# Kernel optimization log

Hardware: AMD Instinct MI355X
Metric: run time of the kernel (lower is better)

The kernel has to match this reference:

```python
import jax, jax.numpy as jnp
import numpy as np

K = 20  # number of top neighbors kept per row
NOISE_SCALE = 1e-4


def setup_inputs() -> dict:
    key = jax.random.key(0)
    k1, k2 = jax.random.split(key)
    B, N = 16, 2048
    A = jax.random.normal(k1, (B, N, N), dtype=jnp.float32)
    noise = jax.random.uniform(k2, (B, N, N), dtype=jnp.float32)
    return {"A": A, "noise": noise}


def reference(A, noise):
    # _activate: ReLU
    A = jax.nn.relu(A)

    # _sparsify: per-row top-k on noise-doped scores, scatter a 0/1 mask, multiply
    A_doped = A + noise * NOISE_SCALE
    _, topk_idx = jax.lax.top_k(A_doped, K)  # (B, N, K)
    B, N, _ = A.shape
    b_idx = jnp.arange(B)[:, None, None]
    r_idx = jnp.arange(N)[None, :, None]
    mask = jnp.zeros_like(A).at[b_idx, r_idx, topk_idx].set(1.0)
    A = A * mask

    # _symmetrize
    A = (A + jnp.swapaxes(A, 1, 2)) * 0.5

    # _normalize ('sym'): A <- D^{-1/2} (A + I) D^{-1/2}
    A = A + jnp.eye(N, dtype=A.dtype)
    d_inv = jnp.sum(A, axis=2) ** -0.5  # (B, N)
    d_inv = jnp.where(jnp.isinf(d_inv), 0.0, d_inv)
    # diag(d) @ A @ diag(d) expressed via broadcasting (same math as batched matmul)
    A = d_inv[:, :, None] * A * d_inv[:, None, :]
    return A
```

## Files before the change

### kernel.cpp

```cpp
#include <hip/hip_runtime.h>

#define NN 2048
#define KK 20
#define BB 16
#define T0F 1.8f
#define CAP 128
#define CSLOT 64

typedef __attribute__((ext_vector_type(4))) float f32x4;

__global__ __launch_bounds__(256, 4) void topk_kernel(
    const float* __restrict__ A, const float* __restrict__ noise,
    int* __restrict__ sel_idx, float* __restrict__ sel_val,
    float* __restrict__ colsum, int* __restrict__ col_cnt,
    unsigned short* __restrict__ col_src)
{
    __shared__ float cand_key[4][CAP];
    __shared__ float cand_val[4][CAP];
    __shared__ int   cand_idx[4][CAP];
    __shared__ int   tie_idx[4][64];
    __shared__ int   tie_cnt[4];

    const int lane = threadIdx.x & 63;
    const int wv   = threadIdx.x >> 6;
    const int row  = blockIdx.x * 4 + wv;
    const float* Ar = A     + (size_t)row * NN;
    const float* Nr = noise + (size_t)row * NN;
    const int colbase = row & ~(NN - 1);
    const unsigned long long ltm = (1ull << lane) - 1ull;

    int*   si = sel_idx + (size_t)row * KK;
    float* sv = sel_val + (size_t)row * KK;

#define EMIT(POS, IDX, V)                                                      \
    do {                                                                       \
        int _p = (POS); int _i = (IDX); float _v = (V);                        \
        si[_p] = _i; sv[_p] = _v;                                              \
        atomicAdd(&colsum[colbase + _i], _v);                                  \
        int _s = atomicAdd(&col_cnt[colbase + _i], 1);                         \
        if (_s < CSLOT)                                                        \
            col_src[(size_t)(colbase + _i) * CSLOT + _s] =                     \
                (unsigned short)(((row & (NN - 1)) << 5) | _p);                \
    } while (0)

    float4 a[8], z[8];
#pragma unroll
    for (int c = 0; c < 8; ++c) a[c] = *(const float4*)(Ar + c * 256 + lane * 4);
#pragma unroll
    for (int c = 0; c < 8; ++c) z[c] = *(const float4*)(Nr + c * 256 + lane * 4);

    int cnt = 0;
#pragma unroll
    for (int c = 0; c < 8; ++c) {
        float av[4] = {a[c].x, a[c].y, a[c].z, a[c].w};
        float nv[4] = {z[c].x, z[c].y, z[c].z, z[c].w};
#pragma unroll
        for (int q = 0; q < 4; ++q) {
            float v = fmaxf(av[q], 0.f);
            float k = v + nv[q] * 1e-4f;
            bool p = k >= T0F;
            unsigned long long m = __ballot(p);
            if (p) {
                int pos = cnt + __popcll(m & ltm);
                if (pos < CAP) {
                    cand_key[wv][pos] = k;
                    cand_val[wv][pos] = v;
                    cand_idx[wv][pos] = c * 256 + lane * 4 + q;
                }
            }
            cnt += __popcll(m);
        }
    }

    bool done = false;
    if (cnt == KK) {
        if (lane < KK)
            EMIT(lane, cand_idx[wv][lane], cand_val[wv][lane]);
        done = true;
    } else if (cnt > KK && cnt <= CAP) {
        float c0 = (lane      < cnt) ? cand_key[wv][lane]      : -1.f;
        float c1 = (lane + 64 < cnt) ? cand_key[wv][lane + 64] : -1.f;

        float mx = fmaxf(c0, c1);
#pragma unroll
        for (int s = 32; s; s >>= 1) mx = fmaxf(mx, __shfl_xor(mx, s));

        unsigned lo = __float_as_uint(T0F);
        unsigned hi = __float_as_uint(mx) + 1u;
        bool exact = false; unsigned tb = 0;
        while (hi - lo > 1u) {
            unsigned mid = (lo + hi) >> 1;
            float tm = __uint_as_float(mid);
            int c = __popcll(__ballot(c0 >= tm)) + __popcll(__ballot(c1 >= tm));
            if (c == KK) { tb = mid; exact = true; break; }
            if (c > KK) lo = mid; else hi = mid;
        }
        if (exact) {
            float t = __uint_as_float(tb);
            bool p = c0 >= t;
            unsigned long long m = __ballot(p);
            if (p) EMIT(__popcll(m & ltm), cand_idx[wv][lane], cand_val[wv][lane]);
            int run = __popcll(m);
            p = c1 >= t;
            m = __ballot(p);
            if (p) EMIT(run + __popcll(m & ltm), cand_idx[wv][lane + 64],
                        cand_val[wv][lane + 64]);
            done = true;
        }
    }

    if (!done) {
        unsigned lo = 0u, hi = 0x7F800000u;
        unsigned tb = 0u;
        bool exact = false;
        while (hi - lo > 1u) {
            unsigned mid = (lo + hi) >> 1;
            float tm = __uint_as_float(mid);
            int c = 0;
            for (int j = 0; j < 32; ++j) {
                float av = Ar[j * 64 + lane];
                float nv = Nr[j * 64 + lane];
                float k = fmaxf(av, 0.f) + nv * 1e-4f;
                c += __popcll(__ballot(k >= tm));
            }
            if (c == KK) { tb = mid; exact = true; break; }
            if (c > KK) lo = mid; else hi = mid;
        }
        if (exact) {
            float t = __uint_as_float(tb);
            int run = 0;
            for (int j = 0; j < 32; ++j) {
                float av = Ar[j * 64 + lane];
                float nv = Nr[j * 64 + lane];
                float v = fmaxf(av, 0.f);
                float k = v + nv * 1e-4f;
                bool p = k >= t;
                unsigned long long m = __ballot(p);
                if (p) EMIT(run + __popcll(m & ltm), j * 64 + lane, v);
                run += __popcll(m);
            }
        } else {
            float t1 = __uint_as_float(lo);
            int run = 0;
            for (int j = 0; j < 32; ++j) {
                float av = Ar[j * 64 + lane];
                float nv = Nr[j * 64 + lane];
                float v = fmaxf(av, 0.f);
                float k = v + nv * 1e-4f;
                bool p = k > t1;
                unsigned long long m = __ballot(p);
                if (p) EMIT(run + __popcll(m & ltm), j * 64 + lane, v);
                run += __popcll(m);
            }
            if (lane == 0) tie_cnt[wv] = 0;
            for (int j = 0; j < 32; ++j) {
                float av = Ar[j * 64 + lane];
                float nv = Nr[j * 64 + lane];
                float k = fmaxf(av, 0.f) + nv * 1e-4f;
                if (k == t1) {
                    int p = atomicAdd(&tie_cnt[wv], 1);
                    if (p < 64) tie_idx[wv][p] = j * 64 + lane;
                }
            }
            if (lane == 0) {
                int n = tie_cnt[wv]; if (n > 64) n = 64;
                int need = KK - run;
                for (int s = 0; s < need; ++s) {
                    int bq = 0, bidx = 0x7fffffff;
                    for (int q = 0; q < n; ++q) {
                        int v = tie_idx[wv][q];
                        if (v < bidx) { bidx = v; bq = q; }
                    }
                    tie_idx[wv][bq] = 0x7fffffff;
                    float v = fmaxf(Ar[bidx], 0.f);
                    EMIT(run + s, bidx, v);
                }
            }
        }
    }
#undef EMIT
}

__global__ __launch_bounds__(256) void dinv_kernel(
    const float* __restrict__ sel_val, const float* __restrict__ colsum,
    float* __restrict__ dinv)
{
    int r = blockIdx.x * 256 + threadIdx.x;
    const float* svp = sel_val + (size_t)r * KK;
    float rs = 0.f;
#pragma unroll
    for (int k = 0; k < KK; ++k) rs += svp[k];
    float d = 1.0f + 0.5f * (rs + colsum[r]);
    dinv[r] = 1.0f / sqrtf(d);
}

__global__ __launch_bounds__(256) void dense_row_kernel(
    const int* __restrict__ sel_idx, const float* __restrict__ sel_val,
    const int* __restrict__ col_cnt, const unsigned short* __restrict__ col_src,
    const float* __restrict__ dinv, float* __restrict__ out)
{
    __shared__ float rowbuf[NN];
    const int r = blockIdx.x;
    const int i = r & (NN - 1);
    const int t = threadIdx.x;
    const int colbase = r & ~(NN - 1);

    float4 zz = {0.f, 0.f, 0.f, 0.f};
#pragma unroll
    for (int c = 0; c < 2; ++c)
        *(float4*)(rowbuf + c * 1024 + t * 4) = zz;
    __syncthreads();

    float di = dinv[r];
    if (t == 0) atomicAdd(&rowbuf[i], di * di);
    if (t < KK) {
        int j  = sel_idx[(size_t)r * KK + t];
        float v = sel_val[(size_t)r * KK + t];
        atomicAdd(&rowbuf[j], 0.5f * v * di * dinv[colbase + j]);
    }
    int cnt = col_cnt[r]; if (cnt > CSLOT) cnt = CSLOT;
    if (t < cnt) {
        unsigned short pk = col_src[(size_t)r * CSLOT + t];
        int srow = pk >> 5, k = pk & 31;
        float v = sel_val[(size_t)(colbase + srow) * KK + k];
        atomicAdd(&rowbuf[srow], 0.5f * v * di * dinv[colbase + srow]);
    }
    __syncthreads();

    size_t base = (size_t)r * NN;
#pragma unroll
    for (int c = 0; c < 2; ++c) {
        int col = c * 1024 + t * 4;
        f32x4 v = *(const f32x4*)(rowbuf + col);
        __builtin_nontemporal_store(v, (f32x4*)(out + base + col));
    }
}

extern "C" void kernel_launch(void* const* d_in, const int* in_sizes, int n_in,
                              void* d_out, int out_size, void* d_ws, size_t ws_size,
                              hipStream_t stream)
{
    const float* A     = (const float*)d_in[0];
    const float* noise = (const float*)d_in[1];
    float* out = (float*)d_out;
    char*  ws  = (char*)d_ws;

    const int rows = BB * NN;
    size_t off = 0;
    int*   sel_idx = (int*)(ws + off);            off += (size_t)rows * KK * 4;
    float* sel_val = (float*)(ws + off);          off += (size_t)rows * KK * 4;
    float* colsum  = (float*)(ws + off);          off += (size_t)rows * 4;
    float* dinv    = (float*)(ws + off);          off += (size_t)rows * 4;
    int*   col_cnt = (int*)(ws + off);            off += (size_t)rows * 4;
    unsigned short* col_src = (unsigned short*)(ws + off);

    hipMemsetAsync(colsum, 0, rows * sizeof(float), stream);
    hipMemsetAsync(col_cnt, 0, rows * sizeof(int), stream);

    topk_kernel<<<rows / 4, 256, 0, stream>>>(A, noise, sel_idx, sel_val,
                                              colsum, col_cnt, col_src);
    dinv_kernel<<<rows / 256, 256, 0, stream>>>(sel_val, colsum, dinv);
    dense_row_kernel<<<rows, 256, 0, stream>>>(sel_idx, sel_val, col_cnt,
                                               col_src, dinv, out);
}
```

Baseline: 700.8 us.

## Prefilter top-k on A alone, gather noise lazily, and batch rows per block

The top-k kernel now screens candidates using only relu(A) against a slightly lowered threshold. It reads noise just for the few surviving indices instead of streaming the whole noise row, which roughly halves the dense input bytes. Each wave handles four rows and prefetches the next row's A while finishing the current one. The dense output kernel processes eight rows per block to amortise launch and setup cost. Candidate compaction now uses LDS atomics, so candidate order is no longer deterministic, and the lowered prefilter threshold must still capture every key above the cutoff.

```diff
diff --git a/kernel.cpp b/kernel.cpp
--- a/kernel.cpp
+++ b/kernel.cpp
@@ -4,33 +4,44 @@
 #define KK 20
 #define BB 16
 #define T0F 1.8f
+#define TPRE (T0F - 1.1e-4f)
 #define CAP 128
 #define CSLOT 64
+#define RPW 4
+#define DRROWS 8
 
 typedef __attribute__((ext_vector_type(4))) float f32x4;
 
-__global__ __launch_bounds__(256, 4) void topk_kernel(
+__global__ __launch_bounds__(256) void topk_kernel(
     const float* __restrict__ A, const float* __restrict__ noise,
     int* __restrict__ sel_idx, float* __restrict__ sel_val,
     float* __restrict__ colsum, int* __restrict__ col_cnt,
     unsigned short* __restrict__ col_src)
 {
-    __shared__ float cand_key[4][CAP];
+    __shared__ int   cand_idx[4][CAP];
     __shared__ float cand_val[4][CAP];
-    __shared__ int   cand_idx[4][CAP];
+    __shared__ int   cand_cnt[4];
     __shared__ int   tie_idx[4][64];
     __shared__ int   tie_cnt[4];
 
     const int lane = threadIdx.x & 63;
     const int wv   = threadIdx.x >> 6;
-    const int row  = blockIdx.x * 4 + wv;
-    const float* Ar = A     + (size_t)row * NN;
-    const float* Nr = noise + (size_t)row * NN;
-    const int colbase = row & ~(NN - 1);
     const unsigned long long ltm = (1ull << lane) - 1ull;
 
-    int*   si = sel_idx + (size_t)row * KK;
-    float* sv = sel_val + (size_t)row * KK;
+    if (lane == 0) cand_cnt[wv] = 0;
+
+    int base = 0;
+
+    {
+        const float* Ar0 = A + (size_t)(blockIdx.x * (4 * RPW) + wv) * NN;
+    }
+    float4 a[8];
+    {
+        const float* Ar0 = A + (size_t)(blockIdx.x * (4 * RPW) + wv) * NN;
+#pragma unroll
+        for (int c = 0; c < 8; ++c)
+            a[c] = *(const float4*)(Ar0 + c * 256 + lane * 4);
+    }
 
 #define EMIT(POS, IDX, V)                                                      \
     do {                                                                       \
@@ -43,137 +54,161 @@
                 (unsigned short)(((row & (NN - 1)) << 5) | _p);                \
     } while (0)
 
-    float4 a[8], z[8];
-#pragma unroll
-    for (int c = 0; c < 8; ++c) a[c] = *(const float4*)(Ar + c * 256 + lane * 4);
-#pragma unroll
-    for (int c = 0; c < 8; ++c) z[c] = *(const float4*)(Nr + c * 256 + lane * 4);
-
-    int cnt = 0;
-#pragma unroll
-    for (int c = 0; c < 8; ++c) {
-        float av[4] = {a[c].x, a[c].y, a[c].z, a[c].w};
-        float nv[4] = {z[c].x, z[c].y, z[c].z, z[c].w};
-#pragma unroll
-        for (int q = 0; q < 4; ++q) {
-            float v = fmaxf(av[q], 0.f);
-            float k = v + nv[q] * 1e-4f;
-            bool p = k >= T0F;
-            unsigned long long m = __ballot(p);
-            if (p) {
-                int pos = cnt + __popcll(m & ltm);
-                if (pos < CAP) {
-                    cand_key[wv][pos] = k;
-                    cand_val[wv][pos] = v;
-                    cand_idx[wv][pos] = c * 256 + lane * 4 + q;
+#pragma unroll
+    for (int rr = 0; rr < RPW; ++rr) {
+        const int row = blockIdx.x * (4 * RPW) + rr * 4 + wv;
+        const float* Ar = A     + (size_t)row * NN;
+        const float* Nr = noise + (size_t)row * NN;
+        const int colbase = row & ~(NN - 1);
+        int*   si = sel_idx + (size_t)row * KK;
+        float* sv = sel_val + (size_t)row * KK;
+
+        int mycnt = 0;
+#pragma unroll
+        for (int c = 0; c < 8; ++c) {
+            float av[4] = {a[c].x, a[c].y, a[c].z, a[c].w};
+#pragma unroll
+            for (int q = 0; q < 4; ++q) {
+                float v = fmaxf(av[q], 0.f);
+                if (v >= TPRE) {
+                    int p = atomicAdd(&cand_cnt[wv], 1) - base;
+                    if (p < CAP) {
+                        cand_idx[wv][p] = c * 256 + lane * 4 + q;
+                        cand_val[wv][p] = v;
+                    }
+                    ++mycnt;
                 }
             }
-            cnt += __popcll(m);
-        }
-    }
-
-    bool done = false;
-    if (cnt == KK) {
-        if (lane < KK)
-            EMIT(lane, cand_idx[wv][lane], cand_val[wv][lane]);
-        done = true;
-    } else if (cnt > KK && cnt <= CAP) {
-        float c0 = (lane      < cnt) ? cand_key[wv][lane]      : -1.f;
-        float c1 = (lane + 64 < cnt) ? cand_key[wv][lane + 64] : -1.f;
-
-        float mx = fmaxf(c0, c1);
-#pragma unroll
-        for (int s = 32; s; s >>= 1) mx = fmaxf(mx, __shfl_xor(mx, s));
-
-        unsigned lo = __float_as_uint(T0F);
-        unsigned hi = __float_as_uint(mx) + 1u;
-        bool exact = false; unsigned tb = 0;
-        while (hi - lo > 1u) {
-            unsigned mid = (lo + hi) >> 1;
-            float tm = __uint_as_float(mid);
-            int c = __popcll(__ballot(c0 >= tm)) + __popcll(__ballot(c1 >= tm));
-            if (c == KK) { tb = mid; exact = true; break; }
-            if (c > KK) lo = mid; else hi = mid;
-        }
-        if (exact) {
-            float t = __uint_as_float(tb);
-            bool p = c0 >= t;
-            unsigned long long m = __ballot(p);
-            if (p) EMIT(__popcll(m & ltm), cand_idx[wv][lane], cand_val[wv][lane]);
-            int run = __popcll(m);
-            p = c1 >= t;
-            m = __ballot(p);
-            if (p) EMIT(run + __popcll(m & ltm), cand_idx[wv][lane + 64],
-                        cand_val[wv][lane + 64]);
-            done = true;
-        }
-    }
-
-    if (!done) {
-        unsigned lo = 0u, hi = 0x7F800000u;
-        unsigned tb = 0u;
-        bool exact = false;
-        while (hi - lo > 1u) {
-            unsigned mid = (lo + hi) >> 1;
-            float tm = __uint_as_float(mid);
-            int c = 0;
-            for (int j = 0; j < 32; ++j) {
-                float av = Ar[j * 64 + lane];
-                float nv = Nr[j * 64 + lane];
-                float k = fmaxf(av, 0.f) + nv * 1e-4f;
-                c += __popcll(__ballot(k >= tm));
+        }
+
+        if (rr + 1 < RPW) {
+            const float* An = A + (size_t)(row + 4) * NN;
+#pragma unroll
+            for (int c = 0; c < 8; ++c)
+                a[c] = *(const float4*)(An + c * 256 + lane * 4);
+        }
+
+        int cnt = mycnt;
+#pragma unroll
+        for (int s = 32; s; s >>= 1) cnt += __shfl_xor(cnt, s);
+        base += cnt;
+
+        bool done = false;
+        if (cnt <= CAP) {
+            int   i0 = (lane      < cnt) ? cand_idx[wv][lane]      : -1;
+            int   i1 = (lane + 64 < cnt) ? cand_idx[wv][lane + 64] : -1;
+            float v0 = (i0 >= 0) ? cand_val[wv][lane]      : 0.f;
+            float v1 = (i1 >= 0) ? cand_val[wv][lane + 64] : 0.f;
+            float k0 = -1.f, k1 = -1.f;
+            if (i0 >= 0) k0 = v0 + Nr[i0] * 1e-4f;
+            if (i1 >= 0) k1 = v1 + Nr[i1] * 1e-4f;
+
+            int cntK = __popcll(__ballot(k0 >= T0F)) +
+                       __popcll(__ballot(k1 >= T0F));
+
+            if (cntK == KK) {
+                bool p = k0 >= T0F;
+                unsigned long long m = __ballot(p);
+                if (p) EMIT(__popcll(m & ltm), i0, v0);
+                int run = __popcll(m);
+                p = k1 >= T0F; m = __ballot(p);
+                if (p) EMIT(run + __popcll(m & ltm), i1, v1);
+                done = true;
+            } else if (cntK > KK) {
+                float mx = fmaxf(k0, k1);
+#pragma unroll
+                for (int s = 32; s; s >>= 1) mx = fmaxf(mx, __shfl_xor(mx, s));
+
+                unsigned lo = __float_as_uint(T0F);
+                unsigned hi = __float_as_uint(mx) + 1u;
+                bool exact = false; unsigned tb = 0;
+                while (hi - lo > 1u) {
+                    unsigned mid = (lo + hi) >> 1;
+                    float tm = __uint_as_float(mid);
+                    int c = __popcll(__ballot(k0 >= tm)) +
+                            __popcll(__ballot(k1 >= tm));
+                    if (c == KK) { tb = mid; exact = true; break; }
+                    if (c > KK) lo = mid; else hi = mid;
+                }
+                if (exact) {
+                    float t = __uint_as_float(tb);
+                    bool p = k0 >= t;
+                    unsigned long long m = __ballot(p);
+                    if (p) EMIT(__popcll(m & ltm), i0, v0);
+                    int run = __popcll(m);
+                    p = k1 >= t; m = __ballot(p);
+                    if (p) EMIT(run + __popcll(m & ltm), i1, v1);
+                    done = true;
+                }
             }
-            if (c == KK) { tb = mid; exact = true; break; }
-            if (c > KK) lo = mid; else hi = mid;
-        }
-        if (exact) {
-            float t = __uint_as_float(tb);
-            int run = 0;
-            for (int j = 0; j < 32; ++j) {
-                float av = Ar[j * 64 + lane];
-                float nv = Nr[j * 64 + lane];
-                float v = fmaxf(av, 0.f);
-                float k = v + nv * 1e-4f;
-                bool p = k >= t;
-                unsigned long long m = __ballot(p);
-                if (p) EMIT(run + __popcll(m & ltm), j * 64 + lane, v);
-                run += __popcll(m);
+        }
+
+        if (!done) {
+            unsigned lo = 0u, hi = 0x7F800000u;
+            unsigned tb = 0u;
+            bool exact = false;
+            while (hi - lo > 1u) {
+                unsigned mid = (lo + hi) >> 1;
+                float tm = __uint_as_float(mid);
+                int c = 0;
+                for (int j = 0; j < 32; ++j) {
+                    float av = Ar[j * 64 + lane];
+                    float nv = Nr[j * 64 + lane];
+                    float k = fmaxf(av, 0.f) + nv * 1e-4f;
+                    c += __popcll(__ballot(k >= tm));
+                }
+                if (c == KK) { tb = mid; exact = true; break; }
+                if (c > KK) lo = mid; else hi = mid;
             }
-        } else {
-            float t1 = __uint_as_float(lo);
-            int run = 0;
-            for (int j = 0; j < 32; ++j) {
-                float av = Ar[j * 64 + lane];
-                float nv = Nr[j * 64 + lane];
-                float v = fmaxf(av, 0.f);
-                float k = v + nv * 1e-4f;
-                bool p = k > t1;
-                unsigned long long m = __ballot(p);
-                if (p) EMIT(run + __popcll(m & ltm), j * 64 + lane, v);
-                run += __popcll(m);
-            }
-            if (lane == 0) tie_cnt[wv] = 0;
-            for (int j = 0; j < 32; ++j) {
-                float av = Ar[j * 64 + lane];
-                float nv = Nr[j * 64 + lane];
-                float k = fmaxf(av, 0.f) + nv * 1e-4f;
-                if (k == t1) {
-                    int p = atomicAdd(&tie_cnt[wv], 1);
-                    if (p < 64) tie_idx[wv][p] = j * 64 + lane;
-                }
-            }
-            if (lane == 0) {
-                int n = tie_cnt[wv]; if (n > 64) n = 64;
-                int need = KK - run;
-                for (int s = 0; s < need; ++s) {
-                    int bq = 0, bidx = 0x7fffffff;
-                    for (int q = 0; q < n; ++q) {
-                        int v = tie_idx[wv][q];
-                        if (v < bidx) { bidx = v; bq = q; }
+            if (exact) {
+                float t = __uint_as_float(tb);
+                int run = 0;
+                for (int j = 0; j < 32; ++j) {
+                    float av = Ar[j * 64 + lane];
+                    float nv = Nr[j * 64 + lane];
+                    float v = fmaxf(av, 0.f);
+                    float k = v + nv * 1e-4f;
+                    bool p = k >= t;
+                    unsigned long long m = __ballot(p);
+                    if (p) EMIT(run + __popcll(m & ltm), j * 64 + lane, v);
+                    run += __popcll(m);
+                }
+            } else {
+                float t1 = __uint_as_float(lo);
+                int run = 0;
+                for (int j = 0; j < 32; ++j) {
+                    float av = Ar[j * 64 + lane];
+                    float nv = Nr[j * 64 + lane];
+                    float v = fmaxf(av, 0.f);
+                    float k = v + nv * 1e-4f;
+                    bool p = k > t1;
+                    unsigned long long m = __ballot(p);
+                    if (p) EMIT(run + __popcll(m & ltm), j * 64 + lane, v);
+                    run += __popcll(m);
+                }
+                if (lane == 0) tie_cnt[wv] = 0;
+                for (int j = 0; j < 32; ++j) {
+                    float av = Ar[j * 64 + lane];
+                    float nv = Nr[j * 64 + lane];
+                    float k = fmaxf(av, 0.f) + nv * 1e-4f;
+                    if (k == t1) {
+                        int p = atomicAdd(&tie_cnt[wv], 1);
+                        if (p < 64) tie_idx[wv][p] = j * 64 + lane;
                     }
-                    tie_idx[wv][bq] = 0x7fffffff;
-                    float v = fmaxf(Ar[bidx], 0.f);
-                    EMIT(run + s, bidx, v);
+                }
+                if (lane == 0) {
+                    int n = tie_cnt[wv]; if (n > 64) n = 64;
+                    int need = KK - run;
+                    for (int s = 0; s < need; ++s) {
+                        int bq = 0, bidx = 0x7fffffff;
+                        for (int q = 0; q < n; ++q) {
+                            int v = tie_idx[wv][q];
+                            if (v < bidx) { bidx = v; bq = q; }
+                        }
+                        tie_idx[wv][bq] = 0x7fffffff;
+                        float v = fmaxf(Ar[bidx], 0.f);
+                        EMIT(run + s, bidx, v);
+                    }
                 }
             }
         }
@@ -200,39 +235,40 @@
     const float* __restrict__ dinv, float* __restrict__ out)
 {
     __shared__ float rowbuf[NN];
-    const int r = blockIdx.x;
-    const int i = r & (NN - 1);
     const int t = threadIdx.x;
-    const int colbase = r & ~(NN - 1);
-
-    float4 zz = {0.f, 0.f, 0.f, 0.f};
-#pragma unroll
-    for (int c = 0; c < 2; ++c)
-        *(float4*)(rowbuf + c * 1024 + t * 4) = zz;
-    __syncthreads();
-
-    float di = dinv[r];
-    if (t == 0) atomicAdd(&rowbuf[i], di * di);
-    if (t < KK) {
-        int j  = sel_idx[(size_t)r * KK + t];
-        float v = sel_val[(size_t)r * KK + t];
-        atomicAdd(&rowbuf[j], 0.5f * v * di * dinv[colbase + j]);
-    }
-    int cnt = col_cnt[r]; if (cnt > CSLOT) cnt = CSLOT;
-    if (t < cnt) {
-        unsigned short pk = col_src[(size_t)r * CSLOT + t];
-        int srow = pk >> 5, k = pk & 31;
-        float v = sel_val[(size_t)(colbase + srow) * KK + k];
-        atomicAdd(&rowbuf[srow], 0.5f * v * di * dinv[colbase + srow]);
-    }
-    __syncthreads();
-
-    size_t base = (size_t)r * NN;
-#pragma unroll
-    for (int c = 0; c < 2; ++c) {
-        int col = c * 1024 + t * 4;
-        f32x4 v = *(const f32x4*)(rowbuf + col);
-        __builtin_nontemporal_store(v, (f32x4*)(out + base + col));
+
+#pragma unroll 1
+    for (int it = 0; it < DRROWS; ++it) {
+        const int r = blockIdx.x * DRROWS + it;
+        const int i = r & (NN - 1);
+        const int colbase = r & ~(NN - 1);
+
+        f32x4 zz = {0.f, 0.f, 0.f, 0.f};
+        *(f32x4*)(rowbuf + t * 4) = zz;
+        *(f32x4*)(rowbuf + 1024 + t * 4) = zz;
+        __syncthreads();
+
+        float di = dinv[r];
+        if (t == 0) atomicAdd(&rowbuf[i], di * di);
+        if (t < KK) {
+            int j  = sel_idx[(size_t)r * KK + t];
+            float v = sel_val[(size_t)r * KK + t];
+            atomicAdd(&rowbuf[j], 0.5f * v * di * dinv[colbase + j]);
+        }
+        int cnt = col_cnt[r]; if (cnt > CSLOT) cnt = CSLOT;
+        if (t < cnt) {
+            unsigned short pk = col_src[(size_t)r * CSLOT + t];
+            int srow = pk >> 5, k = pk & 31;
+            float v = sel_val[(size_t)(colbase + srow) * KK + k];
+            atomicAdd(&rowbuf[srow], 0.5f * v * di * dinv[colbase + srow]);
+        }
+        __syncthreads();
+
+        size_t bb = (size_t)r * NN;
+        f32x4 lo = *(const f32x4*)(rowbuf + t * 4);
+        f32x4 hi = *(const f32x4*)(rowbuf + 1024 + t * 4);
+        __builtin_nontemporal_store(lo, (f32x4*)(out + bb + t * 4));
+        __builtin_nontemporal_store(hi, (f32x4*)(out + bb + 1024 + t * 4));
     }
 }
 
@@ -257,9 +293,9 @@
     hipMemsetAsync(colsum, 0, rows * sizeof(float), stream);
     hipMemsetAsync(col_cnt, 0, rows * sizeof(int), stream);
 
-    topk_kernel<<<rows / 4, 256, 0, stream>>>(A, noise, sel_idx, sel_val,
-                                              colsum, col_cnt, col_src);
+    topk_kernel<<<rows / (4 * RPW), 256, 0, stream>>>(A, noise, sel_idx, sel_val,
+                                                      colsum, col_cnt, col_src);
     dinv_kernel<<<rows / 256, 256, 0, stream>>>(sel_val, colsum, dinv);
-    dense_row_kernel<<<rows, 256, 0, stream>>>(sel_idx, sel_val, col_cnt,
-                                               col_src, dinv, out);
+    dense_row_kernel<<<rows / DRROWS, 256, 0, stream>>>(sel_idx, sel_val, col_cnt,
+                                                        col_src, dinv, out);
 }
```

New measurement: 662.3 us. 1.06x faster.

## Prefilter top-k on A alone, gather noise only for candidates, rank-sort selection

Applied to the files above, without the earlier changes.

The top-k kernel no longer streams the full noise row. It prefilters candidates using only relu(A) against a slightly lowered threshold, gathers noise values just for those candidates, and picks the top K by pairwise rank counting instead of a ballot binary search. This cuts roughly half the dominant global read traffic. In exchange it adds scattered noise gathers and an O(cnt) rank loop. The dense kernel also hoists its index and value loads ahead of the shared-memory zeroing, switches nontemporal stores to plain stores, and drops the occupancy hint from the top-k launch bounds.

```diff
diff --git a/kernel.cpp b/kernel.cpp
--- a/kernel.cpp
+++ b/kernel.cpp
@@ -3,13 +3,13 @@
 #define NN 2048
 #define KK 20
 #define BB 16
-#define T0F 1.8f
+#define TPRE 1.79989f
 #define CAP 128
 #define CSLOT 64
 
 typedef __attribute__((ext_vector_type(4))) float f32x4;
 
-__global__ __launch_bounds__(256, 4) void topk_kernel(
+__global__ __launch_bounds__(256) void topk_kernel(
     const float* __restrict__ A, const float* __restrict__ noise,
     int* __restrict__ sel_idx, float* __restrict__ sel_val,
     float* __restrict__ colsum, int* __restrict__ col_cnt,
@@ -43,27 +43,23 @@
                 (unsigned short)(((row & (NN - 1)) << 5) | _p);                \
     } while (0)
 
-    float4 a[8], z[8];
-#pragma unroll
-    for (int c = 0; c < 8; ++c) a[c] = *(const float4*)(Ar + c * 256 + lane * 4);
-#pragma unroll
-    for (int c = 0; c < 8; ++c) z[c] = *(const float4*)(Nr + c * 256 + lane * 4);
+    float4 a[8];
+#pragma unroll
+    for (int c = 0; c < 8; ++c)
+        a[c] = *(const float4*)(Ar + c * 256 + lane * 4);
 
     int cnt = 0;
 #pragma unroll
     for (int c = 0; c < 8; ++c) {
         float av[4] = {a[c].x, a[c].y, a[c].z, a[c].w};
-        float nv[4] = {z[c].x, z[c].y, z[c].z, z[c].w};
 #pragma unroll
         for (int q = 0; q < 4; ++q) {
             float v = fmaxf(av[q], 0.f);
-            float k = v + nv[q] * 1e-4f;
-            bool p = k >= T0F;
+            bool p = v >= TPRE;
             unsigned long long m = __ballot(p);
             if (p) {
                 int pos = cnt + __popcll(m & ltm);
                 if (pos < CAP) {
-                    cand_key[wv][pos] = k;
                     cand_val[wv][pos] = v;
                     cand_idx[wv][pos] = c * 256 + lane * 4 + q;
                 }
@@ -73,40 +69,27 @@
     }
 
     bool done = false;
-    if (cnt == KK) {
-        if (lane < KK)
-            EMIT(lane, cand_idx[wv][lane], cand_val[wv][lane]);
+    if (cnt >= KK && cnt <= CAP) {
+        int   i0 = (lane      < cnt) ? cand_idx[wv][lane]      : -1;
+        int   i1 = (lane + 64 < cnt) ? cand_idx[wv][lane + 64] : -1;
+        float v0 = (i0 >= 0) ? cand_val[wv][lane]      : 0.f;
+        float v1 = (i1 >= 0) ? cand_val[wv][lane + 64] : 0.f;
+        float k0 = -1.f, k1 = -1.f;
+        if (i0 >= 0) k0 = fmaf(Nr[i0], 1e-4f, v0);
+        if (i1 >= 0) k1 = fmaf(Nr[i1], 1e-4f, v1);
+        cand_key[wv][lane]      = k0;
+        cand_key[wv][lane + 64] = k1;
+
+        int r0 = 0, r1 = 0;
+        for (int j = 0; j < cnt; ++j) {
+            float kj = cand_key[wv][j];
+            int   ij = cand_idx[wv][j];
+            r0 += (kj > k0) || (kj == k0 && ij < i0);
+            r1 += (kj > k1) || (kj == k1 && ij < i1);
+        }
+        if (i0 >= 0 && r0 < KK) EMIT(r0, i0, v0);
+        if (i1 >= 0 && r1 < KK) EMIT(r1, i1, v1);
         done = true;
-    } else if (cnt > KK && cnt <= CAP) {
-        float c0 = (lane      < cnt) ? cand_key[wv][lane]      : -1.f;
-        float c1 = (lane + 64 < cnt) ? cand_key[wv][lane + 64] : -1.f;
-
-        float mx = fmaxf(c0, c1);
-#pragma unroll
-        for (int s = 32; s; s >>= 1) mx = fmaxf(mx, __shfl_xor(mx, s));
-
-        unsigned lo = __float_as_uint(T0F);
-        unsigned hi = __float_as_uint(mx) + 1u;
-        bool exact = false; unsigned tb = 0;
-        while (hi - lo > 1u) {
-            unsigned mid = (lo + hi) >> 1;
-            float tm = __uint_as_float(mid);
-            int c = __popcll(__ballot(c0 >= tm)) + __popcll(__ballot(c1 >= tm));
-            if (c == KK) { tb = mid; exact = true; break; }
-            if (c > KK) lo = mid; else hi = mid;
-        }
-        if (exact) {
-            float t = __uint_as_float(tb);
-            bool p = c0 >= t;
-            unsigned long long m = __ballot(p);
-            if (p) EMIT(__popcll(m & ltm), cand_idx[wv][lane], cand_val[wv][lane]);
-            int run = __popcll(m);
-            p = c1 >= t;
-            m = __ballot(p);
-            if (p) EMIT(run + __popcll(m & ltm), cand_idx[wv][lane + 64],
-                        cand_val[wv][lane + 64]);
-            done = true;
-        }
     }
 
     if (!done) {
@@ -120,7 +103,7 @@
             for (int j = 0; j < 32; ++j) {
                 float av = Ar[j * 64 + lane];
                 float nv = Nr[j * 64 + lane];
-                float k = fmaxf(av, 0.f) + nv * 1e-4f;
+                float k = fmaf(nv, 1e-4f, fmaxf(av, 0.f));
                 c += __popcll(__ballot(k >= tm));
             }
             if (c == KK) { tb = mid; exact = true; break; }
@@ -133,7 +116,7 @@
                 float av = Ar[j * 64 + lane];
                 float nv = Nr[j * 64 + lane];
                 float v = fmaxf(av, 0.f);
-                float k = v + nv * 1e-4f;
+                float k = fmaf(nv, 1e-4f, v);
                 bool p = k >= t;
                 unsigned long long m = __ballot(p);
                 if (p) EMIT(run + __popcll(m & ltm), j * 64 + lane, v);
@@ -146,7 +129,7 @@
                 float av = Ar[j * 64 + lane];
                 float nv = Nr[j * 64 + lane];
                 float v = fmaxf(av, 0.f);
-                float k = v + nv * 1e-4f;
+                float k = fmaf(nv, 1e-4f, v);
                 bool p = k > t1;
                 unsigned long long m = __ballot(p);
                 if (p) EMIT(run + __popcll(m & ltm), j * 64 + lane, v);
@@ -156,7 +139,7 @@
             for (int j = 0; j < 32; ++j) {
                 float av = Ar[j * 64 + lane];
                 float nv = Nr[j * 64 + lane];
-                float k = fmaxf(av, 0.f) + nv * 1e-4f;
+                float k = fmaf(nv, 1e-4f, fmaxf(av, 0.f));
                 if (k == t1) {
                     int p = atomicAdd(&tie_cnt[wv], 1);
                     if (p < 64) tie_idx[wv][p] = j * 64 + lane;
@@ -205,34 +188,39 @@
     const int t = threadIdx.x;
     const int colbase = r & ~(NN - 1);
 
+    float di = dinv[r];
+    int jo = 0; float vo = 0.f, djo = 0.f;
+    if (t < KK) {
+        jo  = sel_idx[(size_t)r * KK + t];
+        vo  = sel_val[(size_t)r * KK + t];
+        djo = dinv[colbase + jo];
+    }
+    int cnt = col_cnt[r]; if (cnt > CSLOT) cnt = CSLOT;
+    int srow = 0; float vi = 0.f, dji = 0.f;
+    if (t < cnt) {
+        unsigned short pk = col_src[(size_t)r * CSLOT + t];
+        srow = pk >> 5;
+        int k = pk & 31;
+        vi  = sel_val[(size_t)(colbase + srow) * KK + k];
+        dji = dinv[colbase + srow];
+    }
+
     float4 zz = {0.f, 0.f, 0.f, 0.f};
 #pragma unroll
     for (int c = 0; c < 2; ++c)
         *(float4*)(rowbuf + c * 1024 + t * 4) = zz;
     __syncthreads();
 
-    float di = dinv[r];
     if (t == 0) atomicAdd(&rowbuf[i], di * di);
-    if (t < KK) {
-        int j  = sel_idx[(size_t)r * KK + t];
-        float v = sel_val[(size_t)r * KK + t];
-        atomicAdd(&rowbuf[j], 0.5f * v * di * dinv[colbase + j]);
-    }
-    int cnt = col_cnt[r]; if (cnt > CSLOT) cnt = CSLOT;
-    if (t < cnt) {
-        unsigned short pk = col_src[(size_t)r * CSLOT + t];
-        int srow = pk >> 5, k = pk & 31;
-        float v = sel_val[(size_t)(colbase + srow) * KK + k];
-        atomicAdd(&rowbuf[srow], 0.5f * v * di * dinv[colbase + srow]);
-    }
+    if (t < KK)  atomicAdd(&rowbuf[jo],   0.5f * vo * di * djo);
+    if (t < cnt) atomicAdd(&rowbuf[srow], 0.5f * vi * di * dji);
     __syncthreads();
 
     size_t base = (size_t)r * NN;
 #pragma unroll
     for (int c = 0; c < 2; ++c) {
         int col = c * 1024 + t * 4;
-        f32x4 v = *(const f32x4*)(rowbuf + col);
-        __builtin_nontemporal_store(v, (f32x4*)(out + base + col));
+        *(float4*)(out + base + col) = *(const float4*)(rowbuf + col);
     }
 }
 
```

New measurement: 641.7 us. 8.4% less time.
